# Kernel optimization log

Hardware: AMD Instinct MI355X
Metric: run time of the kernel (lower is better)

## Reference

```python
import jax, jax.numpy as jnp
import numpy as np

NUM_HEADS = 8
HEAD_DIM = 64
AVG_K_LENGTH = 20
SCALE = 1.0 / (HEAD_DIM ** 0.5 * float(np.log(AVG_K_LENGTH)))  # 1/(sqrt(dim)*log(avg_k_length))


def setup_inputs() -> dict:
    key = jax.random.key(0)
    k1, k2, k3, k4 = jax.random.split(key, 4)
    B, HD, LQ, LK = 4, NUM_HEADS * HEAD_DIM, 2048, 2048
    q = jax.random.normal(k1, (B, HD, LQ), dtype=jnp.float32)
    k = jax.random.normal(k2, (B, HD, LK), dtype=jnp.float32)
    v = jax.random.normal(k3, (B, HD, LK), dtype=jnp.float32)
    k_length = jax.random.randint(k4, (B,), 512, LK + 1, dtype=jnp.int32)
    return {"q": q, "k": k, "v": v, "k_length": k_length}


def reference(q, k, v, k_length):
    b, hd, lq = q.shape
    lk = k.shape[-1]
    d = hd // NUM_HEADS
    # b (h d) l -> b h d l
    qh = q.reshape(b, NUM_HEADS, d, lq)
    kh = k.reshape(b, NUM_HEADS, d, lk)
    vh = v.reshape(b, NUM_HEADS, d, lk)
    # per-batch entropy-invariance scale: scale * log(k_length)
    s = SCALE * jnp.log(k_length.astype(jnp.float32))[:, None, None, None]  # (b,1,1,1)
    attn = jnp.einsum('bhdq,bhdk->bhqk', qh, kh)  # (b,h,lq,lk)
    attn = jax.nn.softmax(s * attn, axis=-1)
    out = jnp.einsum('bhqk,bhdk->bhdq', attn, vh)  # (b,h,d,lq)
    return out.reshape(b, hd, lq)
```

## Files before the change

### kernel.cpp

```cpp
#include <hip/hip_runtime.h>
#include <hip/hip_bf16.h>
#include <math.h>


typedef __attribute__((ext_vector_type(8))) short short8_t;
typedef __attribute__((ext_vector_type(4))) short short4_t;
typedef __attribute__((ext_vector_type(4))) float float4_t;

#define SEQ   2048
#define NBH   32
#define NKT   32

__device__ __forceinline__ unsigned f2bf2u(float a, float b) {
#if __has_builtin(__builtin_amdgcn_cvt_pk_bf16_f32)
  typedef __bf16 bf16x2_t __attribute__((ext_vector_type(2)));
  union { bf16x2_t v; unsigned u; } cv;
  cv.v = __builtin_amdgcn_cvt_pk_bf16_f32(a, b);
  return cv.u;
#else
  union { float f; unsigned u; } x, y;
  x.f = a; y.f = b;
  unsigned ra = x.u + 0x7fffu + ((x.u >> 16) & 1u);
  unsigned rb = y.u + 0x7fffu + ((y.u >> 16) & 1u);
  return (ra >> 16) | (rb & 0xffff0000u);
#endif
}

__device__ __forceinline__ short f2bf1(float a) {
  return (short)(f2bf2u(a, a) & 0xffffu);
}

__device__ __forceinline__ float fast_exp2(float x) {
#if __has_builtin(__builtin_amdgcn_exp2f)
  return __builtin_amdgcn_exp2f(x);
#else
  return exp2f(x);
#endif
}

__device__ __forceinline__ void gld16(const void* g, void* l) {
  __builtin_amdgcn_global_load_lds(
      (const __attribute__((address_space(1))) void*)g,
      (__attribute__((address_space(3))) void*)l, 16, 0, 0);
}

__device__ __forceinline__ float4_t mfma32(short8_t a, short8_t b, float4_t c) {
  return __builtin_amdgcn_mfma_f32_16x16x32_bf16(a, b, c, 0, 0, 0);
}

__device__ __forceinline__ float4_t mfma16(short4_t a, short4_t b, float4_t c) {
#if __has_builtin(__builtin_amdgcn_mfma_f32_16x16x16bf16_1k)
  return __builtin_amdgcn_mfma_f32_16x16x16bf16_1k(a, b, c, 0, 0, 0);
#else
  asm("v_mfma_f32_16x16x16_bf16 %0, %1, %2, %0" : "+v"(c) : "v"(a), "v"(b));
  return c;
#endif
}

#define PST 68
__global__ __launch_bounds__(256, 8)
void eia_prep_kernel(const float* __restrict__ kg, const float* __restrict__ vg,
                     unsigned short* __restrict__ Kt2, unsigned short* __restrict__ Vt2) {
  __shared__ __align__(16) short T[64 * PST];
  const int id  = blockIdx.x;
  const int isV = id >> 10;
  const int sub = id & 1023;
  const int bh  = sub >> 5;
  const int kt  = sub & 31;
  const int t   = threadIdx.x;

  if (!isV) {
    const size_t ib = ((size_t)bh * 64) * SEQ + (size_t)(kt * 64) + (t & 63);
    const int dg = t >> 6;
#pragma unroll
    for (int dd = 0; dd < 16; dd += 4) {
      const int d = dg * 16 + dd;
      const float f0 = kg[ib + (size_t)(d + 0) * SEQ];
      const float f1 = kg[ib + (size_t)(d + 1) * SEQ];
      const float f2 = kg[ib + (size_t)(d + 2) * SEQ];
      const float f3 = kg[ib + (size_t)(d + 3) * SEQ];
      union { short4_t s; unsigned u[2]; } p;
      p.u[0] = f2bf2u(f0, f1);
      p.u[1] = f2bf2u(f2, f3);
      *(short4_t*)&T[(t & 63) * PST + d] = p.s;
    }
    __syncthreads();
    unsigned short* outt = Kt2 + (size_t)(bh * 32 + kt) * 4096;
#pragma unroll
    for (int rep = 0; rep < 2; ++rep) {
      const int id2 = rep * 256 + t;
      const int lr = id2 & 63, ch = id2 >> 6;
      union { short8_t v; short4_t h[2]; } o;
      o.h[0] = *(const short4_t*)&T[lr * PST + ch * 8];
      o.h[1] = *(const short4_t*)&T[lr * PST + ch * 8 + 4];
      *(short8_t*)&outt[ch * 512 + lr * 8] = o.v;
    }
  } else {
#pragma unroll
    for (int rep = 0; rep < 4; ++rep) {
      const int id2 = rep * 256 + t;
      const int d = id2 >> 4, l4 = (id2 & 15) * 4;
      const float4_t f = *(const float4_t*)&vg[((size_t)bh * 64 + d) * SEQ + kt * 64 + l4];
      union { short4_t s; unsigned u[2]; } p;
      p.u[0] = f2bf2u(f[0], f[1]);
      p.u[1] = f2bf2u(f[2], f[3]);
      *(short4_t*)&T[d * PST + l4] = p.s;
    }
    __syncthreads();
    unsigned short* outt = Vt2 + (size_t)(bh * 32 + kt) * 4096;
#pragma unroll
    for (int rep = 0; rep < 2; ++rep) {
      const int c = rep * 256 + t;
      const int k4 = c >> 5, dp = c & 31;
      union { short8_t v; short4_t h[2]; } o;
      o.h[0] = *(const short4_t*)&T[(2 * dp) * PST + k4 * 4];
      o.h[1] = *(const short4_t*)&T[(2 * dp + 1) * PST + k4 * 4];
      *(short8_t*)&outt[k4 * 256 + dp * 8] = o.v;
    }
  }
}

__global__ __launch_bounds__(256, 2)
void eia_attn_kernel(const float* __restrict__ qg,
                     const unsigned short* __restrict__ Kt2,
                     const unsigned short* __restrict__ Vt2,
                     const int* __restrict__ klen,
                     float* __restrict__ outg) {
  __shared__ __align__(16) short SM[24576];

  const int tid  = threadIdx.x;
  const int bh   = blockIdx.x & 31;
  const int qt   = blockIdx.x >> 5;
  const int q0   = qt * 128;
  const int w    = tid >> 6;
  const int lane = tid & 63;
  const int quad = lane >> 4;
  const int l16  = lane & 15;

  const float c = (1.4426950408889634f / (8.0f * 2.9957322735539909f)) *
                  logf((float)klen[bh >> 3]);
  const size_t qb = (size_t)bh * 64 * SEQ;

#pragma unroll
  for (int rep = 0; rep < 8; ++rep) {
    const int id = rep * 256 + tid;
    const int d  = id >> 5;
    const int q4 = (id & 31) * 4;
    const float4_t f = *(const float4_t*)&qg[qb + (size_t)d * SEQ + (size_t)(q0 + q4)];
    SM[(q4 + 0) * 68 + d] = f2bf1(c * f[0]);
    SM[(q4 + 1) * 68 + d] = f2bf1(c * f[1]);
    SM[(q4 + 2) * 68 + d] = f2bf1(c * f[2]);
    SM[(q4 + 3) * 68 + d] = f2bf1(c * f[3]);
  }
  __syncthreads();

  short8_t qfrag[2][2];
#pragma unroll
  for (int g = 0; g < 2; ++g)
#pragma unroll
    for (int s = 0; s < 2; ++s) {
      const short* qp = &SM[(w * 32 + g * 16 + l16) * 68 + s * 32 + quad * 8];
      const short4_t lo = *(const short4_t*)qp;
      const short4_t hi = *(const short4_t*)(qp + 4);
      qfrag[g][s] = short8_t{lo[0], lo[1], lo[2], lo[3], hi[0], hi[1], hi[2], hi[3]};
    }
  __syncthreads();

  const char* ksrc = (const char*)Kt2 + (size_t)bh * NKT * 8192 + (2 * w) * 1024 + lane * 16;
  const char* vsrc = (const char*)Vt2 + (size_t)bh * NKT * 8192 + (2 * w) * 1024 + lane * 16;
  short* const kdst = &SM[(2 * w) * 512];
  short* const vdst = &SM[12288 + (2 * w) * 512];

  const short* const kfp = &SM[quad * 512 + l16 * 8];
  const short* const vfp = &SM[12288 + quad * 256 + l16 * 4];

  const float4_t z4 = {0.f, 0.f, 0.f, 0.f};
  float4_t oacc[2][4];
#pragma unroll
  for (int g = 0; g < 2; ++g)
#pragma unroll
    for (int tt = 0; tt < 4; ++tt) oacc[g][tt] = z4;
  float4_t lacc[2] = {z4, z4};
  const short one_bf = (short)0x3F80;
  const short4_t ones4 = (l16 == 0) ? short4_t{one_bf, one_bf, one_bf, one_bf}
                                    : short4_t{0, 0, 0, 0};

  gld16(ksrc, kdst);              gld16(ksrc + 1024, kdst + 512);
  gld16(vsrc, vdst);              gld16(vsrc + 1024, vdst + 512);
  gld16(ksrc + 8192, kdst + 4096); gld16(ksrc + 8192 + 1024, kdst + 4096 + 512);
  gld16(vsrc + 8192, vdst + 4096); gld16(vsrc + 8192 + 1024, vdst + 4096 + 512);

  int  sc = 0;
  int  sn = 2;
  size_t gsrc = 2 * 8192;

  for (int kt = 0; kt < NKT; ++kt) {
    if (kt < NKT - 1) asm volatile("s_waitcnt vmcnt(4)" ::: "memory");
    else              asm volatile("s_waitcnt vmcnt(0)" ::: "memory");
    asm volatile("s_barrier" ::: "memory");

    if (kt < NKT - 2) {
      const int so = sn * 4096;
      gld16(ksrc + gsrc, kdst + so); gld16(ksrc + gsrc + 1024, kdst + so + 512);
      gld16(vsrc + gsrc, vdst + so); gld16(vsrc + gsrc + 1024, vdst + so + 512);
      gsrc += 8192;
      sn = (sn == 2) ? 0 : sn + 1;
    }
    const int koff = sc * 4096;
    sc = (sc == 2) ? 0 : sc + 1;
    const short* const kb = kfp + koff;
    const short* const vb = vfp + koff;

    float4_t sac[2][4];
#pragma unroll
    for (int t = 0; t < 4; ++t) {
      const short8_t kv = *(const short8_t*)(kb + t * 128);
      sac[0][t] = mfma32(kv, qfrag[0][0], z4);
      sac[1][t] = mfma32(kv, qfrag[1][0], z4);
    }
#pragma unroll
    for (int t = 0; t < 4; ++t) {
      const short8_t kv = *(const short8_t*)(kb + 2048 + t * 128);
      sac[0][t] = mfma32(kv, qfrag[0][1], sac[0][t]);
      sac[1][t] = mfma32(kv, qfrag[1][1], sac[1][t]);
    }

    short4_t pbf[2][4];
#pragma unroll
    for (int g = 0; g < 2; ++g)
#pragma unroll
      for (int t = 0; t < 4; ++t) {
        const float e0 = fast_exp2(sac[g][t][0]);
        const float e1 = fast_exp2(sac[g][t][1]);
        const float e2 = fast_exp2(sac[g][t][2]);
        const float e3 = fast_exp2(sac[g][t][3]);
        union { short4_t s; unsigned u[2]; } p;
        p.u[0] = f2bf2u(e0, e1);
        p.u[1] = f2bf2u(e2, e3);
        pbf[g][t] = p.s;
        lacc[g] = mfma16(ones4, pbf[g][t], lacc[g]);
      }

#pragma unroll
    for (int t = 0; t < 4; ++t) {
      const short* vfb = vb + t * 1024;
#pragma unroll
      for (int tt = 0; tt < 4; ++tt) {
        const short4_t vv = *(const short4_t*)(vfb + tt * 64);
        oacc[0][tt] = mfma16(vv, pbf[0][t], oacc[0][tt]);
        oacc[1][tt] = mfma16(vv, pbf[1][t], oacc[1][tt]);
      }
    }
  }

#pragma unroll
  for (int g = 0; g < 2; ++g) {
    const float ls  = __shfl(lacc[g][0], l16, 64);
    const float inv = 1.0f / ls;
    const size_t ob = qb + (size_t)(q0 + w * 32 + g * 16 + l16);
#pragma unroll
    for (int tt = 0; tt < 4; ++tt)
#pragma unroll
      for (int r = 0; r < 4; ++r)
        outg[ob + (size_t)(tt * 16 + quad * 4 + r) * SEQ] = oacc[g][tt][r] * inv;
  }
}

#define DPAD  72
#define PPAD  68
__global__ __launch_bounds__(256, 5)
void eia_attn_fb(const float* __restrict__ qg, const float* __restrict__ kg,
                 const float* __restrict__ vg, const int* __restrict__ klen,
                 float* __restrict__ outg) {
  __shared__ __align__(16) short QPs[64 * DPAD];
  __shared__ __align__(16) short Ksf[64 * DPAD];
  __shared__ __align__(16) short Vsf[64 * DPAD];

  const int tid  = threadIdx.x;
  const int bh   = blockIdx.x & 31;
  const int qt   = blockIdx.x >> 5;
  const int q0   = qt * 64;
  const int w    = tid >> 6;
  const int lane = tid & 63;
  const int quad = lane >> 4;
  const int l16  = lane & 15;

  const size_t base = (size_t)bh * 64 * SEQ;
  const float c = (1.4426950408889634f / (8.0f * 2.9957322735539909f)) *
                  logf((float)klen[bh >> 3]);

#pragma unroll
  for (int it = 0; it < 2; ++it) {
    const int e = it * 4 + w;
    float f[8];
#pragma unroll
    for (int j = 0; j < 8; ++j)
      f[j] = c * qg[base + (size_t)(e * 8 + j) * SEQ + (size_t)(q0 + lane)];
    union { short8_t s8; unsigned u[4]; } t;
#pragma unroll
    for (int j = 0; j < 4; ++j) t.u[j] = f2bf2u(f[2 * j], f[2 * j + 1]);
    *(short8_t*)&QPs[lane * DPAD + e * 8] = t.s8;
  }
  __syncthreads();

  short8_t qfrag[2];
#pragma unroll
  for (int s = 0; s < 2; ++s)
    qfrag[s] = *(const short8_t*)&QPs[(w * 16 + l16) * DPAD + s * 32 + quad * 8];

  float4_t oacc[4];
#pragma unroll
  for (int t = 0; t < 4; ++t) { oacc[t][0] = 0.f; oacc[t][1] = 0.f; oacc[t][2] = 0.f; oacc[t][3] = 0.f; }
  float lsumv[4] = {0.f, 0.f, 0.f, 0.f};
  const int pbase = w * (16 * DPAD);

  for (int kt = 0; kt < NKT; ++kt) {
    const int k0 = kt * 64;
#pragma unroll
    for (int it = 0; it < 2; ++it) {
      float f[8];
#pragma unroll
      for (int j = 0; j < 8; ++j)
        f[j] = kg[base + (size_t)((it * 4 + w) * 8 + j) * SEQ + (size_t)(k0 + lane)];
      union { short8_t s8; unsigned u[4]; } t;
#pragma unroll
      for (int j = 0; j < 4; ++j) t.u[j] = f2bf2u(f[2 * j], f[2 * j + 1]);
      *(short8_t*)&Ksf[lane * DPAD + (it * 4 + w) * 8] = t.s8;
    }
#pragma unroll
    for (int it = 0; it < 4; ++it) {
      const int d = it * 16 + (w << 2) + (lane >> 4);
      const float4_t vv = *(const float4_t*)&vg[base + (size_t)d * SEQ + (size_t)(k0 + ((lane & 15) << 2))];
      union { short4_t s4; unsigned u[2]; } t;
      t.u[0] = f2bf2u(vv[0], vv[1]);
      t.u[1] = f2bf2u(vv[2], vv[3]);
      *(short4_t*)&Vsf[d * DPAD + ((lane & 15) << 2)] = t.s4;
    }
    __syncthreads();

    float4_t sacc[4];
#pragma unroll
    for (int t = 0; t < 4; ++t) { sacc[t][0] = 0.f; sacc[t][1] = 0.f; sacc[t][2] = 0.f; sacc[t][3] = 0.f; }
#pragma unroll
    for (int t = 0; t < 4; ++t)
#pragma unroll
      for (int s = 0; s < 2; ++s) {
        const short8_t bf = *(const short8_t*)&Ksf[(t * 16 + l16) * DPAD + s * 32 + quad * 8];
        sacc[t] = mfma32(qfrag[s], bf, sacc[t]);
      }

#pragma unroll
    for (int r = 0; r < 4; ++r) {
      const float p0 = fast_exp2(sacc[0][r]);
      const float p1 = fast_exp2(sacc[1][r]);
      const float p2 = fast_exp2(sacc[2][r]);
      const float p3 = fast_exp2(sacc[3][r]);
      lsumv[r] += (p0 + p1) + (p2 + p3);
      const int prow = pbase + (quad * 4 + r) * PPAD + l16;
      QPs[prow +  0] = f2bf1(p0);
      QPs[prow + 16] = f2bf1(p1);
      QPs[prow + 32] = f2bf1(p2);
      QPs[prow + 48] = f2bf1(p3);
    }

#pragma unroll
    for (int s = 0; s < 2; ++s) {
      const short* pr = &QPs[pbase + l16 * PPAD + s * 32 + quad * 8];
      const short4_t plo = *(const short4_t*)pr;
      const short4_t phi = *(const short4_t*)(pr + 4);
      const short8_t pf = {plo[0], plo[1], plo[2], plo[3], phi[0], phi[1], phi[2], phi[3]};
#pragma unroll
      for (int t = 0; t < 4; ++t) {
        const short8_t vf = *(const short8_t*)&Vsf[(t * 16 + l16) * DPAD + s * 32 + quad * 8];
        oacc[t] = mfma32(pf, vf, oacc[t]);
      }
    }
    __syncthreads();
  }

  float inv[4];
#pragma unroll
  for (int r = 0; r < 4; ++r) {
    float v = lsumv[r];
    v += __shfl_xor(v, 1);
    v += __shfl_xor(v, 2);
    v += __shfl_xor(v, 4);
    v += __shfl_xor(v, 8);
    inv[r] = 1.0f / v;
  }
#pragma unroll
  for (int t = 0; t < 4; ++t)
#pragma unroll
    for (int r = 0; r < 4; ++r)
      outg[base + (size_t)(t * 16 + l16) * SEQ +
           (size_t)(q0 + w * 16 + quad * 4 + r)] = oacc[t][r] * inv[r];
}

extern "C" void kernel_launch(void* const* d_in, const int* in_sizes, int n_in,
                              void* d_out, int out_size, void* d_ws, size_t ws_size,
                              hipStream_t stream) {
  const float* q  = (const float*)d_in[0];
  const float* k  = (const float*)d_in[1];
  const float* v  = (const float*)d_in[2];
  const int*   kl = (const int*)d_in[3];
  float* out = (float*)d_out;

  const size_t TEN  = (size_t)NBH * SEQ * 64;
  const size_t need = 2 * TEN * sizeof(unsigned short);

  if (ws_size >= need) {
    unsigned short* Kt2 = (unsigned short*)d_ws;
    unsigned short* Vt2 = Kt2 + TEN;
    eia_prep_kernel<<<2048, 256, 0, stream>>>(k, v, Kt2, Vt2);
    eia_attn_kernel<<<512, 256, 0, stream>>>(q, Kt2, Vt2, kl, out);
  } else {
    eia_attn_fb<<<1024, 256, 0, stream>>>(q, k, v, kl, out);
  }
}
```

Measured before the change: 139.8 us.

## Fuse K/V prep and attention into one cooperative kernel with grid sync

Merges the K/V bf16 transpose prep kernel and the attention kernel into a single cooperative launch. Each of the 512 blocks first does four prep jobs, then waits on a grid-wide barrier before running attention, removing one kernel launch and the gap between the two kernels. Separately, the row-sum of softmax weights moves from an extra MFMA against a ones vector to fp32 VALU adds plus two cross-lane shuffles. The cooperative launch needs all 512 blocks resident at once and falls back to two launches if it fails; the grid barrier itself adds a cost.

```diff
diff --git a/kernel.cpp b/kernel.cpp
--- a/kernel.cpp
+++ b/kernel.cpp
@@ -1,6 +1,9 @@
 #include <hip/hip_runtime.h>
 #include <hip/hip_bf16.h>
+#include <hip/hip_cooperative_groups.h>
 #include <math.h>
+
+namespace cg = cooperative_groups;
 
 
 typedef __attribute__((ext_vector_type(8))) short short8_t;
@@ -58,13 +61,11 @@
 }
 
 #define PST 68
-__global__ __launch_bounds__(256, 8)
-void eia_prep_kernel(const float* __restrict__ kg, const float* __restrict__ vg,
-                     unsigned short* __restrict__ Kt2, unsigned short* __restrict__ Vt2) {
-  __shared__ __align__(16) short T[64 * PST];
-  const int id  = blockIdx.x;
-  const int isV = id >> 10;
-  const int sub = id & 1023;
+__device__ __forceinline__ void prep_job(short* T, const float* kg, const float* vg,
+                                         unsigned short* Kt2, unsigned short* Vt2,
+                                         int job) {
+  const int isV = job >> 10;
+  const int sub = job & 1023;
   const int bh  = sub >> 5;
   const int kt  = sub & 31;
   const int t   = threadIdx.x;
@@ -120,17 +121,13 @@
   }
 }
 
-__global__ __launch_bounds__(256, 2)
-void eia_attn_kernel(const float* __restrict__ qg,
-                     const unsigned short* __restrict__ Kt2,
-                     const unsigned short* __restrict__ Vt2,
-                     const int* __restrict__ klen,
-                     float* __restrict__ outg) {
-  __shared__ __align__(16) short SM[24576];
-
+__device__ __forceinline__ void attn_body(short* SM, const float* qg,
+                                          const unsigned short* Kt2,
+                                          const unsigned short* Vt2,
+                                          const int* klen, float* outg, int bid) {
   const int tid  = threadIdx.x;
-  const int bh   = blockIdx.x & 31;
-  const int qt   = blockIdx.x >> 5;
+  const int bh   = bid & 31;
+  const int qt   = bid >> 5;
   const int q0   = qt * 128;
   const int w    = tid >> 6;
   const int lane = tid & 63;
@@ -180,13 +177,10 @@
   for (int g = 0; g < 2; ++g)
 #pragma unroll
     for (int tt = 0; tt < 4; ++tt) oacc[g][tt] = z4;
-  float4_t lacc[2] = {z4, z4};
-  const short one_bf = (short)0x3F80;
-  const short4_t ones4 = (l16 == 0) ? short4_t{one_bf, one_bf, one_bf, one_bf}
-                                    : short4_t{0, 0, 0, 0};
-
-  gld16(ksrc, kdst);              gld16(ksrc + 1024, kdst + 512);
-  gld16(vsrc, vdst);              gld16(vsrc + 1024, vdst + 512);
+  float lsum[2] = {0.f, 0.f};
+
+  gld16(ksrc, kdst);               gld16(ksrc + 1024, kdst + 512);
+  gld16(vsrc, vdst);               gld16(vsrc + 1024, vdst + 512);
   gld16(ksrc + 8192, kdst + 4096); gld16(ksrc + 8192 + 1024, kdst + 4096 + 512);
   gld16(vsrc + 8192, vdst + 4096); gld16(vsrc + 8192 + 1024, vdst + 4096 + 512);
 
@@ -234,11 +228,11 @@
         const float e1 = fast_exp2(sac[g][t][1]);
         const float e2 = fast_exp2(sac[g][t][2]);
         const float e3 = fast_exp2(sac[g][t][3]);
+        lsum[g] += (e0 + e1) + (e2 + e3);
         union { short4_t s; unsigned u[2]; } p;
         p.u[0] = f2bf2u(e0, e1);
         p.u[1] = f2bf2u(e2, e3);
         pbf[g][t] = p.s;
-        lacc[g] = mfma16(ones4, pbf[g][t], lacc[g]);
       }
 
 #pragma unroll
@@ -255,7 +249,9 @@
 
 #pragma unroll
   for (int g = 0; g < 2; ++g) {
-    const float ls  = __shfl(lacc[g][0], l16, 64);
+    float ls = lsum[g];
+    ls += __shfl_xor(ls, 16);
+    ls += __shfl_xor(ls, 32);
     const float inv = 1.0f / ls;
     const size_t ob = qb + (size_t)(q0 + w * 32 + g * 16 + l16);
 #pragma unroll
@@ -264,6 +260,41 @@
       for (int r = 0; r < 4; ++r)
         outg[ob + (size_t)(tt * 16 + quad * 4 + r) * SEQ] = oacc[g][tt][r] * inv;
   }
+}
+
+__global__ __launch_bounds__(256, 8)
+void eia_prep_kernel(const float* __restrict__ kg, const float* __restrict__ vg,
+                     unsigned short* __restrict__ Kt2, unsigned short* __restrict__ Vt2) {
+  __shared__ __align__(16) short T[64 * PST];
+  prep_job(T, kg, vg, Kt2, Vt2, blockIdx.x);
+}
+
+__global__ __launch_bounds__(256, 2)
+void eia_attn_kernel(const float* __restrict__ qg,
+                     const unsigned short* __restrict__ Kt2,
+                     const unsigned short* __restrict__ Vt2,
+                     const int* __restrict__ klen,
+                     float* __restrict__ outg) {
+  __shared__ __align__(16) short SM[24576];
+  attn_body(SM, qg, Kt2, Vt2, klen, outg, blockIdx.x);
+}
+
+__global__ __launch_bounds__(256, 2)
+void eia_fused_kernel(const float* __restrict__ qg,
+                      const float* __restrict__ kg,
+                      const float* __restrict__ vg,
+                      unsigned short* __restrict__ Kt2,
+                      unsigned short* __restrict__ Vt2,
+                      const int* __restrict__ klen,
+                      float* __restrict__ outg) {
+  __shared__ __align__(16) short SM[24576];
+#pragma unroll
+  for (int i = 0; i < 4; ++i) {
+    prep_job(SM, kg, vg, Kt2, Vt2, blockIdx.x * 4 + i);
+    __syncthreads();
+  }
+  cg::this_grid().sync();
+  attn_body(SM, qg, Kt2, Vt2, klen, outg, blockIdx.x);
 }
 
 #define DPAD  72
@@ -405,14 +436,23 @@
   const int*   kl = (const int*)d_in[3];
   float* out = (float*)d_out;
 
-  const size_t TEN  = (size_t)NBH * SEQ * 64;
-  const size_t need = 2 * TEN * sizeof(unsigned short);
-
-  if (ws_size >= need) {
+  const size_t TEN      = (size_t)NBH * SEQ * 64;
+  const size_t kv_bytes = 2 * TEN * sizeof(unsigned short);
+
+  if (ws_size >= kv_bytes) {
     unsigned short* Kt2 = (unsigned short*)d_ws;
     unsigned short* Vt2 = Kt2 + TEN;
-    eia_prep_kernel<<<2048, 256, 0, stream>>>(k, v, Kt2, Vt2);
-    eia_attn_kernel<<<512, 256, 0, stream>>>(q, Kt2, Vt2, kl, out);
+    const float* qa = q; const float* ka = k; const float* va = v;
+    const int* kla = kl; float* outa = out;
+    unsigned short* Kta = Kt2; unsigned short* Vta = Vt2;
+    void* args[] = {(void*)&qa, (void*)&ka, (void*)&va,
+                    (void*)&Kta, (void*)&Vta, (void*)&kla, (void*)&outa};
+    hipError_t e = hipLaunchCooperativeKernel((const void*)eia_fused_kernel,
+                                              dim3(512), dim3(256), args, 0, stream);
+    if (e != hipSuccess) {
+      eia_prep_kernel<<<2048, 256, 0, stream>>>(k, v, Kt2, Vt2);
+      eia_attn_kernel<<<512, 256, 0, stream>>>(q, Kt2, Vt2, kl, out);
+    }
   } else {
     eia_attn_fb<<<1024, 256, 0, stream>>>(q, k, v, kl, out);
   }
```

Result: slower. 226.1 us (+61.7%).
